# Kernel tuning notes

Hardware: AMD Instinct MI355X
Metric: run time of the kernel (lower is better)

The kernel has to match this reference:

```python
import jax, jax.numpy as jnp
import numpy as np
import math

N = 100000
C = 128
E = 640000
ALPHA = 0.1
THETA = 1.0
LAYER = 4


def setup_inputs() -> dict:
    key = jax.random.key(0)
    k1, k2, k3, k4, k5, k6 = jax.random.split(key, 6)
    x = jax.random.normal(k1, (N, C), dtype=jnp.float32)
    x0 = jax.random.normal(k2, (N, C), dtype=jnp.float32)
    W = jax.random.normal(k3, (C, C), dtype=jnp.float32) / math.sqrt(C)
    b = jax.random.normal(k4, (C,), dtype=jnp.float32) * 0.01
    edge_index = jax.random.randint(k5, (2, E), 0, N, dtype=jnp.int64)
    return {"x": x, "x0": x0, "W": W, "b": b, "edge_index": edge_index}


def _symmetric_propagate(x, edge_index):
    n = x.shape[0]
    loop = jnp.arange(n, dtype=edge_index.dtype)
    src = jnp.concatenate([edge_index[0], loop])  # add self-loops (GCN norm)
    dst = jnp.concatenate([edge_index[1], loop])
    ones = jnp.ones(src.shape[0], dtype=x.dtype)
    deg = jax.ops.segment_sum(ones, dst, num_segments=n)
    dinv = jnp.where(deg > 0, jax.lax.rsqrt(deg), 0.0)
    norm = dinv[src] * dinv[dst]                  # [E+N]
    msgs = x[src] * norm[:, None]                 # gather + scale
    return jax.ops.segment_sum(msgs, dst, num_segments=n)  # scatter-add


def reference(x, x0, W, b, edge_index):
    propagated = _symmetric_propagate(x, edge_index)
    support = (1.0 - ALPHA) * propagated + ALPHA * x0
    beta = math.log(THETA / max(LAYER, 1) + 1.0)
    transformed = support @ W.T + b               # nn.Linear(channels, channels)
    return (1.0 - beta) * support + beta * transformed
```

## Files before the change

### kernel.cpp

```cpp
#include <hip/hip_runtime.h>
#include <stdint.h>

#define C 128
#define ALPHA_F 0.1f
#define ONE_MINUS_ALPHA 0.9f
#define BETA_F 0.22314355131420976f
#define ONE_MINUS_BETA 0.7768564486857902f

typedef __attribute__((ext_vector_type(8))) short bf16x8;
typedef __attribute__((ext_vector_type(4))) float f32x4;

__device__ inline float bf2f(unsigned short u) {
    union { unsigned int i; float f; } c;
    c.i = ((unsigned int)u) << 16;
    return c.f;
}
__device__ inline unsigned short f2bf(float f) {
    union { float f; unsigned int i; } c;
    c.f = f;
    unsigned int r = (c.i + 0x7FFFu + ((c.i >> 16) & 1u)) >> 16;
    return (unsigned short)r;
}

__global__ void k_init(const float* __restrict__ W, unsigned short* __restrict__ Vb,
                       int* __restrict__ cnt, int n) {
    int i = blockIdx.x * 256 + threadIdx.x;
    if (i < n) cnt[i] = 0;
    if (i < C * C) {
        int j = i >> 7;
        int c = i & 127;
        float v = BETA_F * W[i] + ((j == c) ? ONE_MINUS_BETA : 0.f);
        Vb[i] = f2bf(v);
    }
}

__global__ void k_hist(const int* __restrict__ dst, int* __restrict__ cnt,
                       int* __restrict__ rank, int e) {
    int i = blockIdx.x * blockDim.x + threadIdx.x;
    if (i < e) rank[i] = atomicAdd(&cnt[dst[i]], 1);
}

__global__ __launch_bounds__(256)
void k_scan_a(const int* __restrict__ cnt, int* __restrict__ part, int n) {
    __shared__ int s[256];
    int t = threadIdx.x;
    int i = blockIdx.x * 256 + t;
    s[t] = (i < n) ? cnt[i] : 0;
    __syncthreads();
    for (int off = 128; off > 0; off >>= 1) {
        if (t < off) s[t] += s[t + off];
        __syncthreads();
    }
    if (t == 0) part[blockIdx.x] = s[0];
}

__global__ __launch_bounds__(256)
void k_scan_bc(const int* __restrict__ cnt, const int* __restrict__ part,
               int4* __restrict__ meta, int* __restrict__ row_ptr,
               float* __restrict__ dinv, int n) {
    __shared__ int a[256];
    __shared__ int b[256];
    int t   = threadIdx.x;
    int bid = blockIdx.x;

    int local = 0;
    for (int k = t; k < bid; k += 256) local += part[k];
    a[t] = local;
    __syncthreads();
    for (int off = 128; off > 0; off >>= 1) {
        if (t < off) a[t] += a[t + off];
        __syncthreads();
    }
    int blockoff = a[0];
    __syncthreads();

    int i = bid * 256 + t;
    int v = (i < n) ? cnt[i] : 0;
    a[t] = v;
    __syncthreads();
    int* cur = a;
    int* nxt = b;
    for (int off = 1; off < 256; off <<= 1) {
        nxt[t] = cur[t] + ((t >= off) ? cur[t - off] : 0);
        __syncthreads();
        int* tmp = cur; cur = nxt; nxt = tmp;
    }
    if (i < n) {
        int rp = blockoff + cur[t] - v;
        float dv = rsqrtf((float)(v + 1));
        meta[i]    = make_int4(rp, v, __float_as_int(dv), 0);
        row_ptr[i] = rp;
        dinv[i]    = dv;
    }
}

__global__ void k_pl_ybf(const int* __restrict__ src, const int* __restrict__ dst,
                         const int* __restrict__ row_ptr, const int* __restrict__ rank,
                         int* __restrict__ sorted_src, int e,
                         const float* __restrict__ x, const float* __restrict__ dinv,
                         unsigned short* __restrict__ y, int n, int eb) {
    int bid = blockIdx.x;
    if (bid < eb) {
        int i = bid * 256 + threadIdx.x;
        if (i < e) {
            int d = dst[i];
            int pos = row_ptr[d] + rank[i];
            sorted_src[pos] = src[i];
        }
    } else {
        int t = (bid - eb) * 256 + threadIdx.x;
        int total = n * 32;
        if (t < total) {
            int i = t >> 5;
            float dv = dinv[i];
            float4 v = ((const float4*)x)[t];
            ushort4 o;
            o.x = f2bf(v.x * dv);
            o.y = f2bf(v.y * dv);
            o.z = f2bf(v.z * dv);
            o.w = f2bf(v.w * dv);
            ((ushort4*)y)[t] = o;
        }
    }
}

__device__ __forceinline__ float4 acc_node(const ushort4* __restrict__ y4,
                                           const int* __restrict__ ss,
                                           int node, int start, int len,
                                           int eidx, int l32, int base) {
    int m = (len < 32) ? len : 32;
    bool b1 = 1 < m, b2 = 2 < m, b3 = 3 < m;
    bool b4 = 4 < m, b5 = 5 < m, b6 = 6 < m, b7 = 7 < m;
    int s0 = __shfl(eidx, base + 0, 64);
    int s1 = __shfl(eidx, base + (b1 ? 1 : 0), 64);
    int s2 = __shfl(eidx, base + (b2 ? 2 : 0), 64);
    int s3 = __shfl(eidx, base + (b3 ? 3 : 0), 64);
    int s4 = __shfl(eidx, base + (b4 ? 4 : 0), 64);
    int s5 = __shfl(eidx, base + (b5 ? 5 : 0), 64);
    int s6 = __shfl(eidx, base + (b6 ? 6 : 0), 64);
    int s7 = __shfl(eidx, base + (b7 ? 7 : 0), 64);
    ushort4 v0 = y4[(size_t)s0 * 32 + l32];
    ushort4 v1 = y4[(size_t)s1 * 32 + l32];
    ushort4 v2 = y4[(size_t)s2 * 32 + l32];
    ushort4 v3 = y4[(size_t)s3 * 32 + l32];
    ushort4 v4 = y4[(size_t)s4 * 32 + l32];
    ushort4 v5 = y4[(size_t)s5 * 32 + l32];
    ushort4 v6 = y4[(size_t)s6 * 32 + l32];
    ushort4 v7 = y4[(size_t)s7 * 32 + l32];
    ushort4 vs = y4[(size_t)node * 32 + l32];

    float w0 = (0 < m) ? 1.f : 0.f, w1 = b1 ? 1.f : 0.f, w2 = b2 ? 1.f : 0.f, w3 = b3 ? 1.f : 0.f;
    float w4 = b4 ? 1.f : 0.f, w5 = b5 ? 1.f : 0.f, w6 = b6 ? 1.f : 0.f, w7 = b7 ? 1.f : 0.f;

    float4 acc;
    acc.x = bf2f(vs.x) + w0 * bf2f(v0.x) + w1 * bf2f(v1.x) + w2 * bf2f(v2.x) + w3 * bf2f(v3.x)
                       + w4 * bf2f(v4.x) + w5 * bf2f(v5.x) + w6 * bf2f(v6.x) + w7 * bf2f(v7.x);
    acc.y = bf2f(vs.y) + w0 * bf2f(v0.y) + w1 * bf2f(v1.y) + w2 * bf2f(v2.y) + w3 * bf2f(v3.y)
                       + w4 * bf2f(v4.y) + w5 * bf2f(v5.y) + w6 * bf2f(v6.y) + w7 * bf2f(v7.y);
    acc.z = bf2f(vs.z) + w0 * bf2f(v0.z) + w1 * bf2f(v1.z) + w2 * bf2f(v2.z) + w3 * bf2f(v3.z)
                       + w4 * bf2f(v4.z) + w5 * bf2f(v5.z) + w6 * bf2f(v6.z) + w7 * bf2f(v7.z);
    acc.w = bf2f(vs.w) + w0 * bf2f(v0.w) + w1 * bf2f(v1.w) + w2 * bf2f(v2.w) + w3 * bf2f(v3.w)
                       + w4 * bf2f(v4.w) + w5 * bf2f(v5.w) + w6 * bf2f(v6.w) + w7 * bf2f(v7.w);

    for (int j = 8; j < m; j += 4) {
        bool c1 = (j + 1) < m, c2 = (j + 2) < m, c3 = (j + 3) < m;
        int t0 = __shfl(eidx, base + j, 64);
        int t1 = __shfl(eidx, base + (c1 ? j + 1 : j), 64);
        int t2 = __shfl(eidx, base + (c2 ? j + 2 : j), 64);
        int t3 = __shfl(eidx, base + (c3 ? j + 3 : j), 64);
        ushort4 u0 = y4[(size_t)t0 * 32 + l32];
        ushort4 u1 = y4[(size_t)t1 * 32 + l32];
        ushort4 u2 = y4[(size_t)t2 * 32 + l32];
        ushort4 u3 = y4[(size_t)t3 * 32 + l32];
        float q1 = c1 ? 1.f : 0.f, q2 = c2 ? 1.f : 0.f, q3 = c3 ? 1.f : 0.f;
        acc.x += bf2f(u0.x) + q1 * bf2f(u1.x) + q2 * bf2f(u2.x) + q3 * bf2f(u3.x);
        acc.y += bf2f(u0.y) + q1 * bf2f(u1.y) + q2 * bf2f(u2.y) + q3 * bf2f(u3.y);
        acc.z += bf2f(u0.z) + q1 * bf2f(u1.z) + q2 * bf2f(u2.z) + q3 * bf2f(u3.z);
        acc.w += bf2f(u0.w) + q1 * bf2f(u1.w) + q2 * bf2f(u2.w) + q3 * bf2f(u3.w);
    }

    for (int j = 32; j < len; ++j) {
        int t0 = ss[start + j];
        ushort4 u0 = y4[(size_t)t0 * 32 + l32];
        acc.x += bf2f(u0.x);
        acc.y += bf2f(u0.y);
        acc.z += bf2f(u0.z);
        acc.w += bf2f(u0.w);
    }
    return acc;
}

__global__ __launch_bounds__(256)
void k_gather(const unsigned short* __restrict__ y, const float* __restrict__ x0,
              const int* __restrict__ sorted_src, const int4* __restrict__ meta,
              float* __restrict__ soutf, unsigned short* __restrict__ soutb,
              int mode, int n) {
    int tid  = threadIdx.x;
    int l32  = tid & 31;
    int base = tid & 32;
    int hw   = tid >> 5;
    int node0 = blockIdx.x * 16 + hw * 2;
    if (node0 >= n) return;
    int node1 = node0 + 1;
    bool ok1 = node1 < n;
    int vn1 = ok1 ? node1 : node0;

    const ushort4* y4 = (const ushort4*)y;
    const f32x4* x04 = (const f32x4*)x0;

    int4 md0 = meta[node0];
    int4 md1 = meta[vn1];
    int m0 = (md0.y < 32) ? md0.y : 32;
    int m1 = (md1.y < 32) ? md1.y : 32;
    int e0 = (l32 < m0) ? sorted_src[md0.x + l32] : node0;
    int e1 = (l32 < m1) ? sorted_src[md1.x + l32] : vn1;
    f32x4 xv0 = __builtin_nontemporal_load(x04 + (size_t)node0 * 32 + l32);
    f32x4 xv1 = __builtin_nontemporal_load(x04 + (size_t)vn1 * 32 + l32);

    float4 a0 = acc_node(y4, sorted_src, node0, md0.x, md0.y, e0, l32, base);
    float4 a1 = acc_node(y4, sorted_src, vn1,   md1.x, md1.y, e1, l32, base);

    float dv0 = __int_as_float(md0.z);
    float dv1 = __int_as_float(md1.z);

    float4 s0, s1;
    s0.x = ONE_MINUS_ALPHA * (dv0 * a0.x) + ALPHA_F * xv0.x;
    s0.y = ONE_MINUS_ALPHA * (dv0 * a0.y) + ALPHA_F * xv0.y;
    s0.z = ONE_MINUS_ALPHA * (dv0 * a0.z) + ALPHA_F * xv0.z;
    s0.w = ONE_MINUS_ALPHA * (dv0 * a0.w) + ALPHA_F * xv0.w;
    s1.x = ONE_MINUS_ALPHA * (dv1 * a1.x) + ALPHA_F * xv1.x;
    s1.y = ONE_MINUS_ALPHA * (dv1 * a1.y) + ALPHA_F * xv1.y;
    s1.z = ONE_MINUS_ALPHA * (dv1 * a1.z) + ALPHA_F * xv1.z;
    s1.w = ONE_MINUS_ALPHA * (dv1 * a1.w) + ALPHA_F * xv1.w;

    if (mode) {
        unsigned long long p0 =
            (unsigned long long)f2bf(s0.x)
          | ((unsigned long long)f2bf(s0.y) << 16)
          | ((unsigned long long)f2bf(s0.z) << 32)
          | ((unsigned long long)f2bf(s0.w) << 48);
        __builtin_nontemporal_store(
            p0, (unsigned long long*)(soutb + (size_t)node0 * C + l32 * 4));
        if (ok1) {
            unsigned long long p1 =
                (unsigned long long)f2bf(s1.x)
              | ((unsigned long long)f2bf(s1.y) << 16)
              | ((unsigned long long)f2bf(s1.z) << 32)
              | ((unsigned long long)f2bf(s1.w) << 48);
            __builtin_nontemporal_store(
                p1, (unsigned long long*)(soutb + (size_t)node1 * C + l32 * 4));
        }
    } else {
        ((float4*)soutf)[(size_t)node0 * 32 + l32] = s0;
        if (ok1) ((float4*)soutf)[(size_t)node1 * 32 + l32] = s1;
    }
}

__global__ __launch_bounds__(256)
void k_out(const float* __restrict__ sinf, const unsigned short* __restrict__ sinb,
           const unsigned short* __restrict__ Vb, const float* __restrict__ bias,
           float* __restrict__ out, int mode, int n) {
    __shared__ unsigned short wlds[128 * 128];

    int tid  = threadIdx.x;
    int row0 = blockIdx.x * 64;

    const uint4* Vb16 = (const uint4*)Vb;
    for (int i = tid; i < 2048; i += 256) {
        int j = i >> 4;
        int g = i & 15;
        uint4 v = Vb16[i];
        *(uint4*)&wlds[j * 128 + (g ^ (j & 7)) * 8] = v;
    }
    __syncthreads();

    int w    = tid >> 6;
    int lane = tid & 63;
    int l16  = lane & 15;
    int h    = lane >> 4;
    int arow = row0 + w * 16 + l16;
    int arow_c = (arow < n) ? arow : (n - 1);

    f32x4 acc[8];
    #pragma unroll
    for (int t = 0; t < 8; ++t) acc[t] = (f32x4){0.f, 0.f, 0.f, 0.f};

    #pragma unroll
    for (int k0 = 0; k0 < 128; k0 += 32) {
        bf16x8 a;
        if (mode) {
            a = *(const bf16x8*)(sinb + (size_t)arow_c * C + k0 + h * 8);
        } else {
            const float* ap = sinf + (size_t)arow_c * C + k0 + h * 8;
            float4 aa = *(const float4*)ap;
            float4 ab = *(const float4*)(ap + 4);
            union { unsigned short u[8]; bf16x8 v; } pk;
            pk.u[0] = f2bf(aa.x); pk.u[1] = f2bf(aa.y);
            pk.u[2] = f2bf(aa.z); pk.u[3] = f2bf(aa.w);
            pk.u[4] = f2bf(ab.x); pk.u[5] = f2bf(ab.y);
            pk.u[6] = f2bf(ab.z); pk.u[7] = f2bf(ab.w);
            a = pk.v;
        }
        #pragma unroll
        for (int t = 0; t < 8; ++t) {
            int brow = t * 16 + l16;
            int gb = ((k0 >> 3) + h) ^ (brow & 7);
            bf16x8 b = *(const bf16x8*)&wlds[brow * 128 + gb * 8];
            acc[t] = __builtin_amdgcn_mfma_f32_16x16x32_bf16(a, b, acc[t], 0, 0, 0);
        }
    }

    #pragma unroll
    for (int t = 0; t < 8; ++t) {
        int j  = t * 16 + l16;
        float bj = BETA_F * bias[j];
        #pragma unroll
        for (int e2 = 0; e2 < 4; ++e2) {
            int grow = row0 + w * 16 + h * 4 + e2;
            if (grow < n) {
                __builtin_nontemporal_store(acc[t][e2] + bj, &out[(size_t)grow * C + j]);
            }
        }
    }
}

extern "C" void kernel_launch(void* const* d_in, const int* in_sizes, int n_in,
                              void* d_out, int out_size, void* d_ws, size_t ws_size,
                              hipStream_t stream) {
    const float* x   = (const float*)d_in[0];
    const float* x0  = (const float*)d_in[1];
    const float* W   = (const float*)d_in[2];
    const float* b   = (const float*)d_in[3];
    const int*   ei  = (const int*)d_in[4];

    int n = in_sizes[0] / C;
    int e = in_sizes[4] / 2;
    const int* src = ei;
    const int* dst = ei + e;

    int*   cnt        = (int*)d_ws;
    float* dinv       = (float*)(cnt + n);
    int*   part       = (int*)(dinv + n);
    int4*  meta       = (int4*)(part + 512);
    int*   row_ptr    = (int*)(meta + n);
    int*   rank       = row_ptr + n;
    int*   sorted_src = rank + e;
    unsigned short* Vb   = (unsigned short*)(sorted_src + e);
    unsigned short* y    = Vb + C * C;
    unsigned short* sb16 = y + (size_t)n * C;

    size_t need = (size_t)((char*)(sb16 + (size_t)n * C) - (char*)d_ws);
    int mode = (ws_size >= need) ? 1 : 0;

    float* out = (float*)d_out;

    int nb  = (n + 255) / 256;
    int eb  = (e + 255) / 256;
    int ybg = (n * 32 + 255) / 256;

    k_init   <<<nb, 256, 0, stream>>>(W, Vb, cnt, n);
    k_hist   <<<eb, 256, 0, stream>>>(dst, cnt, rank, e);
    k_scan_a <<<nb, 256, 0, stream>>>(cnt, part, n);
    k_scan_bc<<<nb, 256, 0, stream>>>(cnt, part, meta, row_ptr, dinv, n);
    k_pl_ybf <<<eb + ybg, 256, 0, stream>>>(src, dst, row_ptr, rank, sorted_src, e,
                                            x, dinv, y, n, eb);
    k_gather <<<(n + 15) / 16, 256, 0, stream>>>(y, x0, sorted_src, meta,
                                                 out, sb16, mode, n);
    k_out    <<<(n + 63) / 64, 256, 0, stream>>>(out, sb16, Vb, b, out, mode, n);
}
```

Before: 122.9 us.

## Replace CSR build with fixed-slot ELL buckets plus overflow list

Drops the histogram/scan/placement pipeline. Each edge is instead placed directly into a fixed 32-slot per-destination bucket using the atomic rank, and edges past 32 go to a global overflow list that is scanned linearly. dinv is recomputed from counts inline, which removes two kernel launches and the rank and row_ptr traffic. In exchange, sorted_src grows to n*32 ints, and high-degree nodes pay a full linear scan of the overflow list.

```diff
diff --git a/kernel.cpp b/kernel.cpp
--- a/kernel.cpp
+++ b/kernel.cpp
@@ -6,6 +6,7 @@
 #define ONE_MINUS_ALPHA 0.9f
 #define BETA_F 0.22314355131420976f
 #define ONE_MINUS_BETA 0.7768564486857902f
+#define KSLOT 32
 
 typedef __attribute__((ext_vector_type(8))) short bf16x8;
 typedef __attribute__((ext_vector_type(4))) float f32x4;
@@ -23,8 +24,9 @@
 }
 
 __global__ void k_init(const float* __restrict__ W, unsigned short* __restrict__ Vb,
-                       int* __restrict__ cnt, int n) {
+                       int* __restrict__ cnt, int* __restrict__ ovf_cnt, int n) {
     int i = blockIdx.x * 256 + threadIdx.x;
+    if (i == 0) *ovf_cnt = 0;
     if (i < n) cnt[i] = 0;
     if (i < C * C) {
         int j = i >> 7;
@@ -34,101 +36,45 @@
     }
 }
 
-__global__ void k_hist(const int* __restrict__ dst, int* __restrict__ cnt,
-                       int* __restrict__ rank, int e) {
+__global__ void k_hist_place(const int* __restrict__ src, const int* __restrict__ dst,
+                             int* __restrict__ cnt, int* __restrict__ sorted_src,
+                             int* __restrict__ ovf_src, int* __restrict__ ovf_dst,
+                             int* __restrict__ ovf_cnt, int e) {
     int i = blockIdx.x * blockDim.x + threadIdx.x;
-    if (i < e) rank[i] = atomicAdd(&cnt[dst[i]], 1);
-}
-
-__global__ __launch_bounds__(256)
-void k_scan_a(const int* __restrict__ cnt, int* __restrict__ part, int n) {
-    __shared__ int s[256];
-    int t = threadIdx.x;
-    int i = blockIdx.x * 256 + t;
-    s[t] = (i < n) ? cnt[i] : 0;
-    __syncthreads();
-    for (int off = 128; off > 0; off >>= 1) {
-        if (t < off) s[t] += s[t + off];
-        __syncthreads();
-    }
-    if (t == 0) part[blockIdx.x] = s[0];
-}
-
-__global__ __launch_bounds__(256)
-void k_scan_bc(const int* __restrict__ cnt, const int* __restrict__ part,
-               int4* __restrict__ meta, int* __restrict__ row_ptr,
-               float* __restrict__ dinv, int n) {
-    __shared__ int a[256];
-    __shared__ int b[256];
-    int t   = threadIdx.x;
-    int bid = blockIdx.x;
-
-    int local = 0;
-    for (int k = t; k < bid; k += 256) local += part[k];
-    a[t] = local;
-    __syncthreads();
-    for (int off = 128; off > 0; off >>= 1) {
-        if (t < off) a[t] += a[t + off];
-        __syncthreads();
-    }
-    int blockoff = a[0];
-    __syncthreads();
-
-    int i = bid * 256 + t;
-    int v = (i < n) ? cnt[i] : 0;
-    a[t] = v;
-    __syncthreads();
-    int* cur = a;
-    int* nxt = b;
-    for (int off = 1; off < 256; off <<= 1) {
-        nxt[t] = cur[t] + ((t >= off) ? cur[t - off] : 0);
-        __syncthreads();
-        int* tmp = cur; cur = nxt; nxt = tmp;
-    }
-    if (i < n) {
-        int rp = blockoff + cur[t] - v;
-        float dv = rsqrtf((float)(v + 1));
-        meta[i]    = make_int4(rp, v, __float_as_int(dv), 0);
-        row_ptr[i] = rp;
-        dinv[i]    = dv;
-    }
-}
-
-__global__ void k_pl_ybf(const int* __restrict__ src, const int* __restrict__ dst,
-                         const int* __restrict__ row_ptr, const int* __restrict__ rank,
-                         int* __restrict__ sorted_src, int e,
-                         const float* __restrict__ x, const float* __restrict__ dinv,
-                         unsigned short* __restrict__ y, int n, int eb) {
-    int bid = blockIdx.x;
-    if (bid < eb) {
-        int i = bid * 256 + threadIdx.x;
-        if (i < e) {
-            int d = dst[i];
-            int pos = row_ptr[d] + rank[i];
-            sorted_src[pos] = src[i];
-        }
-    } else {
-        int t = (bid - eb) * 256 + threadIdx.x;
-        int total = n * 32;
-        if (t < total) {
-            int i = t >> 5;
-            float dv = dinv[i];
-            float4 v = ((const float4*)x)[t];
-            ushort4 o;
-            o.x = f2bf(v.x * dv);
-            o.y = f2bf(v.y * dv);
-            o.z = f2bf(v.z * dv);
-            o.w = f2bf(v.w * dv);
-            ((ushort4*)y)[t] = o;
-        }
+    if (i < e) {
+        int d = dst[i];
+        int r = atomicAdd(&cnt[d], 1);
+        if (r < KSLOT) {
+            sorted_src[(size_t)d * KSLOT + r] = src[i];
+        } else {
+            int p = atomicAdd(ovf_cnt, 1);
+            ovf_src[p] = src[i];
+            ovf_dst[p] = d;
+        }
+    }
+}
+
+__global__ void k_ybf(const float* __restrict__ x, const int* __restrict__ cnt,
+                      unsigned short* __restrict__ y, int n) {
+    int t = blockIdx.x * 256 + threadIdx.x;
+    int total = n * 32;
+    if (t < total) {
+        int i = t >> 5;
+        float dv = rsqrtf((float)(cnt[i] + 1));
+        float4 v = ((const float4*)x)[t];
+        ushort4 o;
+        o.x = f2bf(v.x * dv);
+        o.y = f2bf(v.y * dv);
+        o.z = f2bf(v.z * dv);
+        o.w = f2bf(v.w * dv);
+        ((ushort4*)y)[t] = o;
     }
 }
 
 __device__ __forceinline__ float4 acc_node(const ushort4* __restrict__ y4,
-                                           const int* __restrict__ ss,
-                                           int node, int start, int len,
+                                           int node, int len,
                                            int eidx, int l32, int base) {
-    int m = (len < 32) ? len : 32;
+    int m = (len < KSLOT) ? len : KSLOT;
     bool b1 = 1 < m, b2 = 2 < m, b3 = 3 < m;
     bool b4 = 4 < m, b5 = 5 < m, b6 = 6 < m, b7 = 7 < m;
     int s0 = __shfl(eidx, base + 0, 64);
@@ -178,21 +124,30 @@
         acc.z += bf2f(u0.z) + q1 * bf2f(u1.z) + q2 * bf2f(u2.z) + q3 * bf2f(u3.z);
         acc.w += bf2f(u0.w) + q1 * bf2f(u1.w) + q2 * bf2f(u2.w) + q3 * bf2f(u3.w);
     }
-
-    for (int j = 32; j < len; ++j) {
-        int t0 = ss[start + j];
-        ushort4 u0 = y4[(size_t)t0 * 32 + l32];
-        acc.x += bf2f(u0.x);
-        acc.y += bf2f(u0.y);
-        acc.z += bf2f(u0.z);
-        acc.w += bf2f(u0.w);
+    return acc;
+}
+
+__device__ __forceinline__ float4 add_ovf(float4 acc, const ushort4* __restrict__ y4,
+                                          const int* __restrict__ ovf_src,
+                                          const int* __restrict__ ovf_dst,
+                                          int oc, int node, int l32) {
+    for (int j = 0; j < oc; ++j) {
+        if (ovf_dst[j] == node) {
+            ushort4 u = y4[(size_t)ovf_src[j] * 32 + l32];
+            acc.x += bf2f(u.x);
+            acc.y += bf2f(u.y);
+            acc.z += bf2f(u.z);
+            acc.w += bf2f(u.w);
+        }
     }
     return acc;
 }
 
 __global__ __launch_bounds__(256)
 void k_gather(const unsigned short* __restrict__ y, const float* __restrict__ x0,
-              const int* __restrict__ sorted_src, const int4* __restrict__ meta,
+              const int* __restrict__ sorted_src, const int* __restrict__ cnt,
+              const int* __restrict__ ovf_src, const int* __restrict__ ovf_dst,
+              const int* __restrict__ ovf_cnt,
               float* __restrict__ soutf, unsigned short* __restrict__ soutb,
               int mode, int n) {
     int tid  = threadIdx.x;
@@ -208,20 +163,26 @@
     const ushort4* y4 = (const ushort4*)y;
     const f32x4* x04 = (const f32x4*)x0;
 
-    int4 md0 = meta[node0];
-    int4 md1 = meta[vn1];
-    int m0 = (md0.y < 32) ? md0.y : 32;
-    int m1 = (md1.y < 32) ? md1.y : 32;
-    int e0 = (l32 < m0) ? sorted_src[md0.x + l32] : node0;
-    int e1 = (l32 < m1) ? sorted_src[md1.x + l32] : vn1;
+    int len0 = cnt[node0];
+    int len1 = cnt[vn1];
+    int m0 = (len0 < KSLOT) ? len0 : KSLOT;
+    int m1 = (len1 < KSLOT) ? len1 : KSLOT;
+    int e0 = (l32 < m0) ? sorted_src[(size_t)node0 * KSLOT + l32] : node0;
+    int e1 = (l32 < m1) ? sorted_src[(size_t)vn1 * KSLOT + l32] : vn1;
     f32x4 xv0 = __builtin_nontemporal_load(x04 + (size_t)node0 * 32 + l32);
     f32x4 xv1 = __builtin_nontemporal_load(x04 + (size_t)vn1 * 32 + l32);
 
-    float4 a0 = acc_node(y4, sorted_src, node0, md0.x, md0.y, e0, l32, base);
-    float4 a1 = acc_node(y4, sorted_src, vn1,   md1.x, md1.y, e1, l32, base);
-
-    float dv0 = __int_as_float(md0.z);
-    float dv1 = __int_as_float(md1.z);
+    float4 a0 = acc_node(y4, node0, len0, e0, l32, base);
+    float4 a1 = acc_node(y4, vn1,   len1, e1, l32, base);
+
+    if (len0 > KSLOT || len1 > KSLOT) {
+        int oc = *ovf_cnt;
+        if (len0 > KSLOT) a0 = add_ovf(a0, y4, ovf_src, ovf_dst, oc, node0, l32);
+        if (len1 > KSLOT) a1 = add_ovf(a1, y4, ovf_src, ovf_dst, oc, vn1, l32);
+    }
+
+    float dv0 = rsqrtf((float)(len0 + 1));
+    float dv1 = rsqrtf((float)(len1 + 1));
 
     float4 s0, s1;
     s0.x = ONE_MINUS_ALPHA * (dv0 * a0.x) + ALPHA_F * xv0.x;
@@ -339,13 +300,11 @@
     const int* dst = ei + e;
 
     int*   cnt        = (int*)d_ws;
-    float* dinv       = (float*)(cnt + n);
-    int*   part       = (int*)(dinv + n);
-    int4*  meta       = (int4*)(part + 512);
-    int*   row_ptr    = (int*)(meta + n);
-    int*   rank       = row_ptr + n;
-    int*   sorted_src = rank + e;
-    unsigned short* Vb   = (unsigned short*)(sorted_src + e);
+    int*   sorted_src = cnt + n;
+    int*   ovf_src    = sorted_src + (size_t)n * KSLOT;
+    int*   ovf_dst    = ovf_src + e;
+    int*   ovf_cnt    = ovf_dst + e;
+    unsigned short* Vb   = (unsigned short*)(ovf_cnt + 16);
     unsigned short* y    = Vb + C * C;
     unsigned short* sb16 = y + (size_t)n * C;
 
@@ -358,13 +317,12 @@
     int eb  = (e + 255) / 256;
     int ybg = (n * 32 + 255) / 256;
 
-    k_init   <<<nb, 256, 0, stream>>>(W, Vb, cnt, n);
-    k_hist   <<<eb, 256, 0, stream>>>(dst, cnt, rank, e);
-    k_scan_a <<<nb, 256, 0, stream>>>(cnt, part, n);
-    k_scan_bc<<<nb, 256, 0, stream>>>(cnt, part, meta, row_ptr, dinv, n);
-    k_pl_ybf <<<eb + ybg, 256, 0, stream>>>(src, dst, row_ptr, rank, sorted_src, e,
-                                            x, dinv, y, n, eb);
-    k_gather <<<(n + 15) / 16, 256, 0, stream>>>(y, x0, sorted_src, meta,
-                                                 out, sb16, mode, n);
-    k_out    <<<(n + 63) / 64, 256, 0, stream>>>(out, sb16, Vb, b, out, mode, n);
-}
+    k_init      <<<nb, 256, 0, stream>>>(W, Vb, cnt, ovf_cnt, n);
+    k_hist_place<<<eb, 256, 0, stream>>>(src, dst, cnt, sorted_src,
+                                         ovf_src, ovf_dst, ovf_cnt, e);
+    k_ybf       <<<ybg, 256, 0, stream>>>(x, cnt, y, n);
+    k_gather    <<<(n + 15) / 16, 256, 0, stream>>>(y, x0, sorted_src, cnt,
+                                                    ovf_src, ovf_dst, ovf_cnt,
+                                                    out, sb16, mode, n);
+    k_out       <<<(n + 63) / 64, 256, 0, stream>>>(out, sb16, Vb, b, out, mode, n);
+}
```

After: 121.6 us. About the same (-1.0%).
